# Kernel tuning notes

Hardware: AMD Instinct MI355X
Metric: run time of the kernel (lower is better)

The kernel has to match this reference:

```python
import jax, jax.numpy as jnp
import numpy as np

D_MODEL, D_HEAD, D_MLP, N_HEADS = 768, 64, 3072, 12
BATCH, SEQ = 1, 4096
LN_EPS = 1e-05
IGNORE = -100000.0


def setup_inputs() -> dict:
    key = jax.random.key(0)
    ks = jax.random.split(key, 8)
    s = 0.02
    return {
        "resid_pre": jax.random.normal(ks[0], (BATCH, SEQ, D_MODEL), jnp.float32),
        "ln1_w": jnp.ones((D_MODEL,), jnp.float32),
        "ln1_b": jnp.zeros((D_MODEL,), jnp.float32),
        "ln2_w": jnp.ones((D_MODEL,), jnp.float32),
        "ln2_b": jnp.zeros((D_MODEL,), jnp.float32),
        "W_Q": jax.random.normal(ks[1], (N_HEADS, D_MODEL, D_HEAD), jnp.float32) * s,
        "W_K": jax.random.normal(ks[2], (N_HEADS, D_MODEL, D_HEAD), jnp.float32) * s,
        "W_V": jax.random.normal(ks[3], (N_HEADS, D_MODEL, D_HEAD), jnp.float32) * s,
        "W_O": jax.random.normal(ks[4], (N_HEADS, D_HEAD, D_MODEL), jnp.float32) * s,
        "b_Q": jnp.zeros((N_HEADS, D_HEAD), jnp.float32),
        "b_K": jnp.zeros((N_HEADS, D_HEAD), jnp.float32),
        "b_V": jnp.zeros((N_HEADS, D_HEAD), jnp.float32),
        "b_O": jnp.zeros((D_MODEL,), jnp.float32),
        "W_in": jax.random.normal(ks[5], (D_MODEL, D_MLP), jnp.float32) * s,
        "b_in": jnp.zeros((D_MLP,), jnp.float32),
        "W_out": jax.random.normal(ks[6], (D_MLP, D_MODEL), jnp.float32) * s,
        "b_out": jnp.zeros((D_MODEL,), jnp.float32),
    }


def _layernorm(x, w, b):
    mean = jnp.mean(x, axis=-1, keepdims=True)
    var = jnp.var(x, axis=-1, keepdims=True)  # unbiased=False
    return (x - mean) * jax.lax.rsqrt(var + LN_EPS) * w + b


def _attention(x, W_Q, W_K, W_V, W_O, b_Q, b_K, b_V, b_O):
    # x: [b, s, d_model]; W_{Q,K,V}: [h, d_model, d_head]
    q = jnp.einsum("bsm,hmd->bshd", x, W_Q) + b_Q
    k = jnp.einsum("bsm,hmd->bshd", x, W_K) + b_K
    v = jnp.einsum("bsm,hmd->bshd", x, W_V) + b_V
    scores = jnp.einsum("bqhd,bkhd->bhqk", q, k) / np.sqrt(D_HEAD).astype(np.float32)
    seq = x.shape[1]
    causal = jnp.tril(jnp.ones((seq, seq), bool))  # True where allowed
    scores = jnp.where(causal, scores, IGNORE)
    pattern = jax.nn.softmax(scores, axis=-1)
    z = jnp.einsum("bkhd,bhqk->bqhd", v, pattern)
    return jnp.einsum("bqhd,hdm->bqm", z, W_O) + b_O


def reference(resid_pre, ln1_w, ln1_b, ln2_w, ln2_b,
              W_Q, W_K, W_V, W_O, b_Q, b_K, b_V, b_O,
              W_in, b_in, W_out, b_out):
    resid_mid = _attention(_layernorm(resid_pre, ln1_w, ln1_b),
                           W_Q, W_K, W_V, W_O, b_Q, b_K, b_V, b_O) + resid_pre
    pre = jnp.einsum("bsm,mf->bsf", _layernorm(resid_mid, ln2_w, ln2_b), W_in) + b_in
    post = jax.nn.gelu(pre, approximate=False)  # torch F.gelu default = exact erf
    mlp_out = jnp.einsum("bsf,fm->bsm", post, W_out) + b_out
    resid_post = mlp_out + resid_mid
    return (resid_post, post)
```

## Files before the change

### kernel.cpp

```cpp
#include <hip/hip_runtime.h>
#include <hip/hip_bf16.h>
#include <math.h>

using bf16 = __hip_bfloat16;
using u16  = unsigned short;
using u32  = unsigned int;
using short8 = __attribute__((ext_vector_type(8))) short;
using f32x4  = __attribute__((ext_vector_type(4))) float;

#define AS1 __attribute__((address_space(1)))
#define AS3 __attribute__((address_space(3)))

__device__ __forceinline__ void gld_lds16(const void* g, void* l) {
  __builtin_amdgcn_global_load_lds((const AS1 u32*)g, (AS3 u32*)l, 16, 0, 0);
}

__device__ __forceinline__ bool probe_f32(const void* p) {
  return *(const u32*)p == 0x3F800000u;
}
__device__ __forceinline__ float ldf(const void* p, size_t i, bool f32) {
  return f32 ? ((const float*)p)[i] : __bfloat162float(((const bf16*)p)[i]);
}
__device__ __forceinline__ void stf(void* p, size_t i, float v, bool f32) {
  if (f32) ((float*)p)[i] = v;
  else     ((bf16*)p)[i] = __float2bfloat16(v);
}
__device__ __forceinline__ u16 bfbits(float x) {
  bf16 h = __float2bfloat16(x);
  u16 b; __builtin_memcpy(&b, &h, 2); return b;
}

__global__ __launch_bounds__(256) void ln_kernel(const void* __restrict__ x,
    const void* __restrict__ w, const void* __restrict__ b, bf16* __restrict__ out,
    const void* probe, int x_is_f32)
{
  const bool pf = probe_f32(probe);
  const bool xf = x_is_f32 ? true : pf;
  const int row = blockIdx.x, t = threadIdx.x;
  const size_t base = (size_t)row * 768;
  float v[3]; float s1 = 0.f, s2 = 0.f;
#pragma unroll
  for (int i = 0; i < 3; ++i) { float f = ldf(x, base + i*256 + t, xf); v[i] = f; s1 += f; s2 += f*f; }
#pragma unroll
  for (int off = 32; off >= 1; off >>= 1) { s1 += __shfl_xor(s1, off); s2 += __shfl_xor(s2, off); }
  __shared__ float a1[4], a2[4];
  if ((t & 63) == 0) { a1[t>>6] = s1; a2[t>>6] = s2; }
  __syncthreads();
  float S1 = a1[0]+a1[1]+a1[2]+a1[3];
  float S2 = a2[0]+a2[1]+a2[2]+a2[3];
  float mean = S1 * (1.f/768.f);
  float var  = S2 * (1.f/768.f) - mean*mean;
  float rs = rsqrtf(var + 1e-5f);
#pragma unroll
  for (int i = 0; i < 3; ++i) {
    int c = i*256 + t;
    out[base + c] = __float2bfloat16((v[i]-mean)*rs*ldf(w, c, pf) + ldf(b, c, pf));
  }
}

__global__ __launch_bounds__(256) void prep_all(
    const void* W_Q, const void* W_K, const void* W_V, const void* Wo,
    const void* Win, const void* Wout,
    const void* bQ, const void* bK, const void* bV, const void* bO,
    const void* bIn, const void* bOut,
    bf16* __restrict__ qkvT, bf16* __restrict__ WoT, bf16* __restrict__ WinT,
    bf16* __restrict__ WoutT, float* __restrict__ biasA, const void* probe)
{
  const bool pf = probe_f32(probe);
  const int bid = blockIdx.x;
  if (bid >= 6912) {
    int i = (bid - 6912)*256 + threadIdx.x;
    float v;
    if (i < 2304)      v = (i < 768) ? ldf(bQ, i, pf) : (i < 1536 ? ldf(bK, i-768, pf) : ldf(bV, i-1536, pf));
    else if (i < 3072) v = ldf(bO, i-2304, pf);
    else if (i < 6144) v = ldf(bIn, i-3072, pf);
    else               v = ldf(bOut, i-6144, pf);
    biasA[i] = v;
    return;
  }
  const void* src; bf16* dst; int R, C, bx, by; size_t soff = 0;
  if (bid < 1728) {
    int mtx = bid / 576, within = bid % 576;
    int h = within / 48, t = within % 48;
    by = t >> 1; bx = t & 1;
    src = (mtx == 0) ? W_Q : (mtx == 1 ? W_K : W_V);
    soff = (size_t)h * 49152;
    dst = qkvT + ((size_t)mtx*768 + h*64) * 768;
    R = 768; C = 64;
  } else if (bid < 2304) {
    int within = bid - 1728; bx = within % 24; by = within / 24;
    src = Wo; dst = WoT; R = 768; C = 768;
  } else if (bid < 4608) {
    int within = bid - 2304; bx = within % 96; by = within / 96;
    src = Win; dst = WinT; R = 768; C = 3072;
  } else {
    int within = bid - 4608; bx = within % 24; by = within / 24;
    src = Wout; dst = WoutT; R = 3072; C = 768;
  }
  __shared__ bf16 tile[32][33];
  const int bc = bx*32, br = by*32;
  const int tx = threadIdx.x & 31, ty = threadIdx.x >> 5;
#pragma unroll
  for (int i = 0; i < 32; i += 8)
    tile[ty+i][tx] = __float2bfloat16(ldf(src, soff + (size_t)(br+ty+i)*C + bc + tx, pf));
  __syncthreads();
#pragma unroll
  for (int i = 0; i < 32; i += 8)
    dst[(size_t)(bc+ty+i)*R + br + tx] = tile[tx][ty+i];
}

template<int MODE, int BM, int BN>
__global__ __launch_bounds__(256) void gemm_bt(const bf16* __restrict__ A,
    const bf16* __restrict__ BT, const float* __restrict__ bias,
    const void* __restrict__ res, void* __restrict__ Cout, bf16* __restrict__ aux,
    size_t outOff, const void* probe, int M, int N, int K,
    float* __restrict__ zf, float* __restrict__ sf)
{
  constexpr int MR = BM/32, NR = BN/32;
  __shared__ bf16 Alds[BM*64];
  __shared__ bf16 Blds[BN*64];
  const int tid = threadIdx.x;
  const int lane = tid & 63, w = tid >> 6;
  const int l15 = lane & 15, l4 = lane >> 4;

  if (MODE == 0) {
    int bid = blockIdx.y * gridDim.x + blockIdx.x;
    float4 z4 = {0.f, 0.f, 0.f, 0.f};
    float4* zp = (float4*)zf + (size_t)bid*1024;
#pragma unroll
    for (int i = 0; i < 4; ++i) zp[i*256 + tid] = z4;
    if (tid < 16) ((float4*)sf)[bid*16 + tid] = z4;
  }

  const int brow = blockIdx.y * BM, bcol = blockIdx.x * BN;
  const int wr = (w >> 1) * (BM/2), wc = (w & 1) * (BN/2);
  const bf16* Ag = A  + (size_t)brow * K;
  const bf16* Bg = BT + (size_t)bcol * K;
  f32x4 acc[MR][NR];
#pragma unroll
  for (int i = 0; i < MR; ++i)
#pragma unroll
    for (int j = 0; j < NR; ++j) acc[i][j] = 0.f;

  for (int kt = 0; kt < K; kt += 64) {
#pragma unroll
    for (int i = 0; i < BM/32; ++i) {
      int id = i*256 + tid, r = id >> 3;
      int sw = (r ^ (r >> 3)) & 7;
      int csrc = ((id & 7) ^ sw) * 8;
      gld_lds16(Ag + (size_t)r*K + kt + csrc, (char*)Alds + id*16);
    }
#pragma unroll
    for (int i = 0; i < BN/32; ++i) {
      int id = i*256 + tid, r = id >> 3;
      int sw = (r ^ (r >> 3)) & 7;
      int csrc = ((id & 7) ^ sw) * 8;
      gld_lds16(Bg + (size_t)r*K + kt + csrc, (char*)Blds + id*16);
    }
    __syncthreads();
#pragma unroll
    for (int kk = 0; kk < 2; ++kk) {
      short8 a[MR], b[NR];
#pragma unroll
      for (int mi = 0; mi < MR; ++mi) {
        int row = wr + mi*16 + l15, sw = (row ^ (row >> 3)) & 7;
        a[mi] = *(const short8*)((const char*)Alds + row*128 + (((kk*4 + l4) ^ sw) << 4));
      }
#pragma unroll
      for (int ni = 0; ni < NR; ++ni) {
        int row = wc + ni*16 + l15, sw = (row ^ (row >> 3)) & 7;
        b[ni] = *(const short8*)((const char*)Blds + row*128 + (((kk*4 + l4) ^ sw) << 4));
      }
      __builtin_amdgcn_s_setprio(1);
#pragma unroll
      for (int mi = 0; mi < MR; ++mi)
#pragma unroll
        for (int ni = 0; ni < NR; ++ni)
          acc[mi][ni] = __builtin_amdgcn_mfma_f32_16x16x32_bf16(a[mi], b[ni], acc[mi][ni], 0, 0, 0);
      __builtin_amdgcn_s_setprio(0);
    }
    __syncthreads();
  }

  const bool pf = probe_f32(probe);
#pragma unroll
  for (int mi = 0; mi < MR; ++mi) {
#pragma unroll
    for (int r = 0; r < 4; ++r) {
      int row = brow + wr + mi*16 + l4*4 + r;
      size_t rowoff = (size_t)row * N;
#pragma unroll
      for (int ni = 0; ni < NR; ++ni) {
        int col = bcol + wc + ni*16 + l15;
        float v = acc[mi][ni][r] + bias[col];
        if (MODE == 1) v += ldf(res, rowoff + col, pf);
        if (MODE == 3) v += ((const float*)res)[rowoff + col];
        if (MODE == 2) v = 0.5f * v * (1.0f + erff(v * 0.70710678118654752f));
        if (MODE == 0) ((bf16*)Cout)[rowoff + col] = __float2bfloat16(v);
        else if (MODE == 1) ((float*)Cout)[rowoff + col] = v;
        else {
          stf(Cout, outOff + rowoff + col, v, pf);
          if (MODE == 2) aux[rowoff + col] = __float2bfloat16(v);
        }
      }
    }
  }
}

__global__ __launch_bounds__(256) void attn_kernel(const bf16* __restrict__ QKV,
    float* __restrict__ Zf, float* __restrict__ Sf)
{
  __shared__ bf16 Qs[4096];
  __shared__ bf16 Ks[2][4096];
  __shared__ bf16 VTs[2][4096];
  __shared__ bf16 Ps[4][1024];
  const int cid = 159 - blockIdx.x, h = blockIdx.y;
  int qb, c;
  if (cid < 16)      { qb = cid;                    c = 0; }
  else if (cid < 48) { qb = 16 + ((cid-16) >> 1);   c = (cid-16) & 1; }
  else if (cid < 96) { qb = 32 + (cid-48)/3;        c = (cid-48)%3; }
  else               { qb = 48 + ((cid-96) >> 2);   c = (cid-96) & 3; }
  const int t_lo = c*16, t_hi = min(c*16 + 16, qb + 1);

  const int tid = threadIdx.x, lane = tid & 63, w = tid >> 6;
  const int l15 = lane & 15, l4 = lane >> 4;
  const int q0 = qb * 64;

  const int vw = tid >> 3, vd0 = (tid & 7) * 8;
  const int vk0 = (vw >> 1) + (vw & 1) * 32;
  uint4 va, vb;

#pragma unroll
  for (int i = 0; i < 2; ++i) {
    int id = i*256 + tid, r = id >> 3;
    int s = (r ^ (r >> 3)) & 7;
    int csrc = ((id & 7) ^ s) * 8;
    gld_lds16(QKV + (size_t)(q0 + r)*2304 + h*64 + csrc, (char*)Qs + id*16);
    gld_lds16(QKV + (size_t)(t_lo*64 + r)*2304 + 768 + h*64 + csrc, (char*)Ks[0] + id*16);
  }
  va = *(const uint4*)(QKV + (size_t)(t_lo*64 + vk0)*2304 + 1536 + h*64 + vd0);
  vb = *(const uint4*)(QKV + (size_t)(t_lo*64 + vk0 + 16)*2304 + 1536 + h*64 + vd0);
  {
    const u16* pa = (const u16*)&va; const u16* pb = (const u16*)&vb;
#pragma unroll
    for (int d = 0; d < 8; ++d) {
      int row = vd0 + d, srow = (row ^ (row >> 3)) & 7;
      int addr = row*128 + (((vw >> 2) ^ srow) << 4) + (vw & 3)*4;
      *(u32*)((char*)VTs[0] + addr) = (u32)pa[d] | ((u32)pb[d] << 16);
    }
  }
  __syncthreads();

  f32x4 o[4]; f32x4 osum;
#pragma unroll
  for (int dt = 0; dt < 4; ++dt) o[dt] = 0.f;
  osum = 0.f;
  short8 ones8;
#pragma unroll
  for (int j = 0; j < 8; ++j) ones8[j] = 0x3F80;

  for (int nt = t_lo; nt < t_hi; ++nt) {
    const int cur = (nt - t_lo) & 1, nxt = cur ^ 1;
    if (nt + 1 < t_hi) {
      const int t0n = (nt + 1) * 64;
#pragma unroll
      for (int i = 0; i < 2; ++i) {
        int id = i*256 + tid, r = id >> 3;
        int s = (r ^ (r >> 3)) & 7;
        int csrc = ((id & 7) ^ s) * 8;
        gld_lds16(QKV + (size_t)(t0n + r)*2304 + 768 + h*64 + csrc, (char*)Ks[nxt] + id*16);
      }
      va = *(const uint4*)(QKV + (size_t)(t0n + vk0)*2304 + 1536 + h*64 + vd0);
      vb = *(const uint4*)(QKV + (size_t)(t0n + vk0 + 16)*2304 + 1536 + h*64 + vd0);
    }

    f32x4 s4[4];
#pragma unroll
    for (int ct = 0; ct < 4; ++ct) s4[ct] = 0.f;
    const int qrow = w*16 + l15, sq = (qrow ^ (qrow >> 3)) & 7;
    __builtin_amdgcn_s_setprio(1);
#pragma unroll
    for (int kk = 0; kk < 2; ++kk) {
      short8 aq = *(const short8*)((const char*)Qs + qrow*128 + (((kk*4 + l4) ^ sq) << 4));
#pragma unroll
      for (int ct = 0; ct < 4; ++ct) {
        int krow = ct*16 + l15, sk = (krow ^ (krow >> 3)) & 7;
        short8 bk = *(const short8*)((const char*)Ks[cur] + krow*128 + (((kk*4 + l4) ^ sk) << 4));
        s4[ct] = __builtin_amdgcn_mfma_f32_16x16x32_bf16(aq, bk, s4[ct], 0, 0, 0);
      }
    }
    __builtin_amdgcn_s_setprio(0);

    const bool diag = (nt == qb);
#pragma unroll
    for (int r = 0; r < 4; ++r) {
      const int prow = l4*4 + r, sp = (prow ^ (prow >> 3)) & 7;
      float p[4];
#pragma unroll
      for (int ct = 0; ct < 4; ++ct) {
        float sv = s4[ct][r] * 0.125f;
        if (diag && (ct*16 + l15 > w*16 + l4*4 + r)) sv = -100000.0f;
        p[ct] = __expf(fminf(sv, 30.0f));
      }
      uint2 pk;
      pk.x = (u32)bfbits(p[0]) | ((u32)bfbits(p[1]) << 16);
      pk.y = (u32)bfbits(p[2]) | ((u32)bfbits(p[3]) << 16);
      *(uint2*)((char*)&Ps[w][0] + prow*128 + (((l15 >> 1) ^ sp) << 4) + (l15 & 1)*8) = pk;
    }

    const int prow2 = l15, sp2 = (prow2 ^ (prow2 >> 3)) & 7;
    __builtin_amdgcn_s_setprio(1);
#pragma unroll
    for (int kg = 0; kg < 2; ++kg) {
      short8 ap = *(const short8*)((const char*)&Ps[w][0] + prow2*128 + (((kg*4 + l4) ^ sp2) << 4));
#pragma unroll
      for (int dt = 0; dt < 4; ++dt) {
        int vrow2 = dt*16 + l15, sv2 = (vrow2 ^ (vrow2 >> 3)) & 7;
        short8 bv = *(const short8*)((const char*)VTs[cur] + vrow2*128 + (((kg*4 + l4) ^ sv2) << 4));
        o[dt] = __builtin_amdgcn_mfma_f32_16x16x32_bf16(ap, bv, o[dt], 0, 0, 0);
      }
      osum = __builtin_amdgcn_mfma_f32_16x16x32_bf16(ap, ones8, osum, 0, 0, 0);
    }
    __builtin_amdgcn_s_setprio(0);

    if (nt + 1 < t_hi) {
      const u16* pa = (const u16*)&va; const u16* pb = (const u16*)&vb;
#pragma unroll
      for (int d = 0; d < 8; ++d) {
        int row = vd0 + d, srow = (row ^ (row >> 3)) & 7;
        int addr = row*128 + (((vw >> 2) ^ srow) << 4) + (vw & 3)*4;
        *(u32*)((char*)VTs[nxt] + addr) = (u32)pa[d] | ((u32)pb[d] << 16);
      }
    }
    __syncthreads();
  }

  const int qrow0 = q0 + w*16 + l4*4;
#pragma unroll
  for (int r = 0; r < 4; ++r)
    if (l15 == 0) unsafeAtomicAdd(&Sf[(size_t)h*4096 + qrow0 + r], osum[r]);
#pragma unroll
  for (int dt = 0; dt < 4; ++dt)
#pragma unroll
    for (int r = 0; r < 4; ++r)
      unsafeAtomicAdd(&Zf[(size_t)(qrow0 + r)*768 + h*64 + dt*16 + l15], o[dt][r]);
}

__global__ __launch_bounds__(256) void norm_z(const float* __restrict__ Zf,
    const float* __restrict__ Sf, bf16* __restrict__ Zb)
{
  const int row = blockIdx.x, t = threadIdx.x;
  const size_t base = (size_t)row * 768;
#pragma unroll
  for (int i = 0; i < 3; ++i) {
    int cx = i*256 + t;
    int hh = cx >> 6;
    Zb[base + cx] = __float2bfloat16(Zf[base + cx] * __builtin_amdgcn_rcpf(Sf[(size_t)hh*4096 + row]));
  }
}

extern "C" void kernel_launch(void* const* d_in, const int* in_sizes, int n_in,
                              void* d_out, int out_size, void* d_ws, size_t ws_size,
                              hipStream_t stream)
{
  (void)in_sizes; (void)n_in; (void)out_size; (void)ws_size;
  const void* resid_pre = d_in[0];
  const void* ln1_w = d_in[1];
  const void* ln1_b = d_in[2];
  const void* ln2_w = d_in[3];
  const void* ln2_b = d_in[4];
  const void* W_Q  = d_in[5];
  const void* W_K  = d_in[6];
  const void* W_V  = d_in[7];
  const void* W_O  = d_in[8];
  const void* b_Q  = d_in[9];
  const void* b_K  = d_in[10];
  const void* b_V  = d_in[11];
  const void* b_O  = d_in[12];
  const void* W_in  = d_in[13];
  const void* b_in  = d_in[14];
  const void* W_out = d_in[15];
  const void* b_out = d_in[16];
  const void* probe = ln1_w;

  char* ws = (char*)d_ws;
  bf16*  qkvT  = (bf16*)(ws + 0);
  bf16*  WoT   = (bf16*)(ws + 3538944);
  bf16*  WinT  = (bf16*)(ws + 4718592);
  bf16*  WoutT = (bf16*)(ws + 9437184);
  float* biasA = (float*)(ws + 14155776);
  bf16*  x1    = (bf16*)(ws + 14183424);
  bf16*  QKV   = (bf16*)(ws + 20474880);
  bf16*  Zb    = (bf16*)(ws + 39349248);
  float* mid   = (float*)(ws + 45640704);
  bf16*  x2    = (bf16*)(ws + 58223616);
  bf16*  postB = (bf16*)(ws + 20474880);
  float* Zf    = (float*)(ws + 45640704);
  float* Sf    = (float*)(ws + 58223616);

  prep_all<<<6939, 256, 0, stream>>>(W_Q, W_K, W_V, W_O, W_in, W_out,
      b_Q, b_K, b_V, b_O, b_in, b_out, qkvT, WoT, WinT, WoutT, biasA, probe);

  ln_kernel<<<4096, 256, 0, stream>>>(resid_pre, ln1_w, ln1_b, x1, probe, 0);
  gemm_bt<0,128,96><<<dim3(24,32), 256, 0, stream>>>(x1, qkvT, biasA, nullptr, QKV, nullptr, 0, probe, 4096, 2304, 768, Zf, Sf);
  attn_kernel<<<dim3(160,12), 256, 0, stream>>>(QKV, Zf, Sf);
  norm_z<<<4096, 256, 0, stream>>>(Zf, Sf, Zb);
  gemm_bt<1,64,64><<<dim3(12,64), 256, 0, stream>>>(Zb, WoT, biasA+2304, resid_pre, mid, nullptr, 0, probe, 4096, 768, 768, nullptr, nullptr);
  ln_kernel<<<4096, 256, 0, stream>>>(mid, ln2_w, ln2_b, x2, probe, 1);
  gemm_bt<2,128,128><<<dim3(24,32), 256, 0, stream>>>(x2, WinT, biasA+3072, nullptr, d_out, postB, 3145728, probe, 4096, 3072, 768, nullptr, nullptr);
  gemm_bt<3,64,64><<<dim3(12,64), 256, 0, stream>>>(postB, WoutT, biasA+6144, mid, d_out, nullptr, 0, probe, 4096, 768, 3072, nullptr, nullptr);
}
```

Measured before the change: 236.7 us.

## Double-buffer GEMM LDS tiles with configurable BK; keep Q in registers in attention

The GEMM kernel now double-buffers its A/B LDS tiles, prefetching the next K-slice while MFMAs run on the current one. BK becomes a template parameter, with a 32-wide variant and a different swizzle for the large-tile GEMMs to keep LDS usage bounded. Attention now holds Q fragments in registers instead of LDS and single-buffers V^T using explicit barriers, which frees LDS and may raise occupancy. The softmax uses exp2 with a prescaled log2e constant. The manual waitcnt/barrier placement adds a risk of ordering bugs.

```diff
diff --git a/kernel.cpp b/kernel.cpp
--- a/kernel.cpp
+++ b/kernel.cpp
@@ -13,6 +13,11 @@
 
 __device__ __forceinline__ void gld_lds16(const void* g, void* l) {
   __builtin_amdgcn_global_load_lds((const AS1 u32*)g, (AS3 u32*)l, 16, 0, 0);
+}
+__device__ __forceinline__ void raw_barrier() {
+  __builtin_amdgcn_sched_barrier(0);
+  __builtin_amdgcn_s_barrier();
+  __builtin_amdgcn_sched_barrier(0);
 }
 
 __device__ __forceinline__ bool probe_f32(const void* p) {
@@ -109,7 +114,7 @@
     dst[(size_t)(bc+ty+i)*R + br + tx] = tile[tx][ty+i];
 }
 
-template<int MODE, int BM, int BN>
+template<int MODE, int BM, int BN, int BK>
 __global__ __launch_bounds__(256) void gemm_bt(const bf16* __restrict__ A,
     const bf16* __restrict__ BT, const float* __restrict__ bias,
     const void* __restrict__ res, void* __restrict__ Cout, bf16* __restrict__ aux,
@@ -117,8 +122,9 @@
     float* __restrict__ zf, float* __restrict__ sf)
 {
   constexpr int MR = BM/32, NR = BN/32;
-  __shared__ bf16 Alds[BM*64];
-  __shared__ bf16 Blds[BN*64];
+  constexpr int CH = BK/8;
+  __shared__ bf16 Alds[2][BM*BK];
+  __shared__ bf16 Blds[2][BN*BK];
   const int tid = threadIdx.x;
   const int lane = tid & 63, w = tid >> 6;
   const int l15 = lane & 15, l4 = lane >> 4;
@@ -142,34 +148,46 @@
 #pragma unroll
     for (int j = 0; j < NR; ++j) acc[i][j] = 0.f;
 
-  for (int kt = 0; kt < K; kt += 64) {
-#pragma unroll
-    for (int i = 0; i < BM/32; ++i) {
-      int id = i*256 + tid, r = id >> 3;
-      int sw = (r ^ (r >> 3)) & 7;
-      int csrc = ((id & 7) ^ sw) * 8;
-      gld_lds16(Ag + (size_t)r*K + kt + csrc, (char*)Alds + id*16);
-    }
-#pragma unroll
-    for (int i = 0; i < BN/32; ++i) {
-      int id = i*256 + tid, r = id >> 3;
-      int sw = (r ^ (r >> 3)) & 7;
-      int csrc = ((id & 7) ^ sw) * 8;
-      gld_lds16(Bg + (size_t)r*K + kt + csrc, (char*)Blds + id*16);
-    }
-    __syncthreads();
-#pragma unroll
-    for (int kk = 0; kk < 2; ++kk) {
+  auto swzf = [](int r) { return BK == 64 ? ((r ^ (r >> 3)) & 7) : ((r >> 1) & 3); };
+  auto STAGE = [&](int bb, int kt) {
+#pragma unroll
+    for (int i = 0; i < (BM*CH + 255)/256; ++i) {
+      int id = i*256 + tid;
+      if ((BM*CH % 256) == 0 || id < BM*CH) {
+        int r = id / CH, cc = id % CH;
+        gld_lds16(Ag + (size_t)r*K + kt + ((cc ^ swzf(r)) * 8), (char*)Alds[bb] + id*16);
+      }
+    }
+#pragma unroll
+    for (int i = 0; i < (BN*CH + 255)/256; ++i) {
+      int id = i*256 + tid;
+      if ((BN*CH % 256) == 0 || id < BN*CH) {
+        int r = id / CH, cc = id % CH;
+        gld_lds16(Bg + (size_t)r*K + kt + ((cc ^ swzf(r)) * 8), (char*)Blds[bb] + id*16);
+      }
+    }
+  };
+
+  STAGE(0, 0);
+  asm volatile("s_waitcnt vmcnt(0)" ::: "memory");
+  raw_barrier();
+
+  const int nIt = K / BK;
+  for (int it = 0; it < nIt; ++it) {
+    const int cur = it & 1;
+    if (it + 1 < nIt) STAGE(cur ^ 1, (it + 1) * BK);
+#pragma unroll
+    for (int kk = 0; kk < BK/32; ++kk) {
       short8 a[MR], b[NR];
 #pragma unroll
       for (int mi = 0; mi < MR; ++mi) {
-        int row = wr + mi*16 + l15, sw = (row ^ (row >> 3)) & 7;
-        a[mi] = *(const short8*)((const char*)Alds + row*128 + (((kk*4 + l4) ^ sw) << 4));
+        int row = wr + mi*16 + l15;
+        a[mi] = *(const short8*)((const char*)Alds[cur] + row*(BK*2) + (((kk*4 + l4) ^ swzf(row)) << 4));
       }
 #pragma unroll
       for (int ni = 0; ni < NR; ++ni) {
-        int row = wc + ni*16 + l15, sw = (row ^ (row >> 3)) & 7;
-        b[ni] = *(const short8*)((const char*)Blds + row*128 + (((kk*4 + l4) ^ sw) << 4));
+        int row = wc + ni*16 + l15;
+        b[ni] = *(const short8*)((const char*)Blds[cur] + row*(BK*2) + (((kk*4 + l4) ^ swzf(row)) << 4));
       }
       __builtin_amdgcn_s_setprio(1);
 #pragma unroll
@@ -179,7 +197,9 @@
           acc[mi][ni] = __builtin_amdgcn_mfma_f32_16x16x32_bf16(a[mi], b[ni], acc[mi][ni], 0, 0, 0);
       __builtin_amdgcn_s_setprio(0);
     }
-    __syncthreads();
+    __builtin_amdgcn_sched_barrier(0);
+    asm volatile("s_waitcnt vmcnt(0) lgkmcnt(0)" ::: "memory");
+    raw_barrier();
   }
 
   const bool pf = probe_f32(probe);
@@ -210,9 +230,8 @@
 __global__ __launch_bounds__(256) void attn_kernel(const bf16* __restrict__ QKV,
     float* __restrict__ Zf, float* __restrict__ Sf)
 {
-  __shared__ bf16 Qs[4096];
   __shared__ bf16 Ks[2][4096];
-  __shared__ bf16 VTs[2][4096];
+  __shared__ bf16 VTs[4096];
   __shared__ bf16 Ps[4][1024];
   const int cid = 159 - blockIdx.x, h = blockIdx.y;
   int qb, c;
@@ -230,12 +249,16 @@
   const int vk0 = (vw >> 1) + (vw & 1) * 32;
   uint4 va, vb;
 
+  short8 qf[2];
+#pragma unroll
+  for (int kk = 0; kk < 2; ++kk)
+    qf[kk] = *(const short8*)(QKV + (size_t)(q0 + w*16 + l15)*2304 + h*64 + kk*32 + l4*8);
+
 #pragma unroll
   for (int i = 0; i < 2; ++i) {
     int id = i*256 + tid, r = id >> 3;
     int s = (r ^ (r >> 3)) & 7;
     int csrc = ((id & 7) ^ s) * 8;
-    gld_lds16(QKV + (size_t)(q0 + r)*2304 + h*64 + csrc, (char*)Qs + id*16);
     gld_lds16(QKV + (size_t)(t_lo*64 + r)*2304 + 768 + h*64 + csrc, (char*)Ks[0] + id*16);
   }
   va = *(const uint4*)(QKV + (size_t)(t_lo*64 + vk0)*2304 + 1536 + h*64 + vd0);
@@ -246,7 +269,7 @@
     for (int d = 0; d < 8; ++d) {
       int row = vd0 + d, srow = (row ^ (row >> 3)) & 7;
       int addr = row*128 + (((vw >> 2) ^ srow) << 4) + (vw & 3)*4;
-      *(u32*)((char*)VTs[0] + addr) = (u32)pa[d] | ((u32)pb[d] << 16);
+      *(u32*)((char*)VTs + addr) = (u32)pa[d] | ((u32)pb[d] << 16);
     }
   }
   __syncthreads();
@@ -261,7 +284,8 @@
 
   for (int nt = t_lo; nt < t_hi; ++nt) {
     const int cur = (nt - t_lo) & 1, nxt = cur ^ 1;
-    if (nt + 1 < t_hi) {
+    const bool pref = (nt + 1 < t_hi);
+    if (pref) {
       const int t0n = (nt + 1) * 64;
 #pragma unroll
       for (int i = 0; i < 2; ++i) {
@@ -277,16 +301,14 @@
     f32x4 s4[4];
 #pragma unroll
     for (int ct = 0; ct < 4; ++ct) s4[ct] = 0.f;
-    const int qrow = w*16 + l15, sq = (qrow ^ (qrow >> 3)) & 7;
     __builtin_amdgcn_s_setprio(1);
 #pragma unroll
     for (int kk = 0; kk < 2; ++kk) {
-      short8 aq = *(const short8*)((const char*)Qs + qrow*128 + (((kk*4 + l4) ^ sq) << 4));
 #pragma unroll
       for (int ct = 0; ct < 4; ++ct) {
         int krow = ct*16 + l15, sk = (krow ^ (krow >> 3)) & 7;
         short8 bk = *(const short8*)((const char*)Ks[cur] + krow*128 + (((kk*4 + l4) ^ sk) << 4));
-        s4[ct] = __builtin_amdgcn_mfma_f32_16x16x32_bf16(aq, bk, s4[ct], 0, 0, 0);
+        s4[ct] = __builtin_amdgcn_mfma_f32_16x16x32_bf16(qf[kk], bk, s4[ct], 0, 0, 0);
       }
     }
     __builtin_amdgcn_s_setprio(0);
@@ -298,9 +320,9 @@
       float p[4];
 #pragma unroll
       for (int ct = 0; ct < 4; ++ct) {
-        float sv = s4[ct][r] * 0.125f;
-        if (diag && (ct*16 + l15 > w*16 + l4*4 + r)) sv = -100000.0f;
-        p[ct] = __expf(fminf(sv, 30.0f));
+        float sv = s4[ct][r] * 0.18033688f;
+        if (diag && (ct*16 + l15 > w*16 + l4*4 + r)) sv = -30000.0f;
+        p[ct] = exp2f(fminf(sv, 43.0f));
       }
       uint2 pk;
       pk.x = (u32)bfbits(p[0]) | ((u32)bfbits(p[1]) << 16);
@@ -316,23 +338,29 @@
 #pragma unroll
       for (int dt = 0; dt < 4; ++dt) {
         int vrow2 = dt*16 + l15, sv2 = (vrow2 ^ (vrow2 >> 3)) & 7;
-        short8 bv = *(const short8*)((const char*)VTs[cur] + vrow2*128 + (((kg*4 + l4) ^ sv2) << 4));
+        short8 bv = *(const short8*)((const char*)VTs + vrow2*128 + (((kg*4 + l4) ^ sv2) << 4));
         o[dt] = __builtin_amdgcn_mfma_f32_16x16x32_bf16(ap, bv, o[dt], 0, 0, 0);
       }
       osum = __builtin_amdgcn_mfma_f32_16x16x32_bf16(ap, ones8, osum, 0, 0, 0);
     }
     __builtin_amdgcn_s_setprio(0);
 
-    if (nt + 1 < t_hi) {
+    __builtin_amdgcn_sched_barrier(0);
+    asm volatile("s_waitcnt lgkmcnt(0)" ::: "memory");
+    raw_barrier();
+
+    if (pref) {
       const u16* pa = (const u16*)&va; const u16* pb = (const u16*)&vb;
 #pragma unroll
       for (int d = 0; d < 8; ++d) {
         int row = vd0 + d, srow = (row ^ (row >> 3)) & 7;
         int addr = row*128 + (((vw >> 2) ^ srow) << 4) + (vw & 3)*4;
-        *(u32*)((char*)VTs[nxt] + addr) = (u32)pa[d] | ((u32)pb[d] << 16);
-      }
-    }
-    __syncthreads();
+        *(u32*)((char*)VTs + addr) = (u32)pa[d] | ((u32)pb[d] << 16);
+      }
+    }
+    __builtin_amdgcn_sched_barrier(0);
+    asm volatile("s_waitcnt vmcnt(0) lgkmcnt(0)" ::: "memory");
+    raw_barrier();
   }
 
   const int qrow0 = q0 + w*16 + l4*4;
@@ -402,11 +430,11 @@
       b_Q, b_K, b_V, b_O, b_in, b_out, qkvT, WoT, WinT, WoutT, biasA, probe);
 
   ln_kernel<<<4096, 256, 0, stream>>>(resid_pre, ln1_w, ln1_b, x1, probe, 0);
-  gemm_bt<0,128,96><<<dim3(24,32), 256, 0, stream>>>(x1, qkvT, biasA, nullptr, QKV, nullptr, 0, probe, 4096, 2304, 768, Zf, Sf);
+  gemm_bt<0,128,96,32><<<dim3(24,32), 256, 0, stream>>>(x1, qkvT, biasA, nullptr, QKV, nullptr, 0, probe, 4096, 2304, 768, Zf, Sf);
   attn_kernel<<<dim3(160,12), 256, 0, stream>>>(QKV, Zf, Sf);
   norm_z<<<4096, 256, 0, stream>>>(Zf, Sf, Zb);
-  gemm_bt<1,64,64><<<dim3(12,64), 256, 0, stream>>>(Zb, WoT, biasA+2304, resid_pre, mid, nullptr, 0, probe, 4096, 768, 768, nullptr, nullptr);
+  gemm_bt<1,64,64,64><<<dim3(12,64), 256, 0, stream>>>(Zb, WoT, biasA+2304, resid_pre, mid, nullptr, 0, probe, 4096, 768, 768, nullptr, nullptr);
   ln_kernel<<<4096, 256, 0, stream>>>(mid, ln2_w, ln2_b, x2, probe, 1);
-  gemm_bt<2,128,128><<<dim3(24,32), 256, 0, stream>>>(x2, WinT, biasA+3072, nullptr, d_out, postB, 3145728, probe, 4096, 3072, 768, nullptr, nullptr);
-  gemm_bt<3,64,64><<<dim3(12,64), 256, 0, stream>>>(postB, WoutT, biasA+6144, mid, d_out, nullptr, 0, probe, 4096, 768, 3072, nullptr, nullptr);
-}
+  gemm_bt<2,128,128,32><<<dim3(24,32), 256, 0, stream>>>(x2, WinT, biasA+3072, nullptr, d_out, postB, 3145728, probe, 4096, 3072, 768, nullptr, nullptr);
+  gemm_bt<3,64,64,64><<<dim3(12,64), 256, 0, stream>>>(postB, WoutT, biasA+6144, mid, d_out, nullptr, 0, probe, 4096, 768, 3072, nullptr, nullptr);
+}
```

Result: slower. 249.9 us (+5.6%).
